# Kernel optimization log

Measured on AMD Instinct MI355X. Metric: run time of the kernel, lower is better.

## Reference

```python
import jax, jax.numpy as jnp
import numpy as np

N, E, IN_DIM, H, D = 40000, 640000, 128, 8, 16


def setup_inputs() -> dict:
    key = jax.random.key(0)
    k_h, k_s, k_d, k_q, k_k, k_v = jax.random.split(key, 6)
    scale = float(np.sqrt(2.0 / (IN_DIM + H * D)))  # xavier-ish
    return {
        "h": jax.random.normal(k_h, (N, IN_DIM), dtype=jnp.float32),
        "src": jax.random.randint(k_s, (E,), 0, N, dtype=jnp.int32),
        "dst": jax.random.randint(k_d, (E,), 0, N, dtype=jnp.int32),
        "WQ": jax.random.normal(k_q, (IN_DIM, H * D), dtype=jnp.float32) * scale,
        "WK": jax.random.normal(k_k, (IN_DIM, H * D), dtype=jnp.float32) * scale,
        "WV": jax.random.normal(k_v, (IN_DIM, H * D), dtype=jnp.float32) * scale,
    }


def reference(h, src, dst, WQ, WK, WV):
    n = h.shape[0]
    Q = (h @ WQ).reshape(n, H, D)  # [N,H,D]
    K = (h @ WK).reshape(n, H, D)
    V = (h @ WV).reshape(n, H, D)
    inv_sqrt_d = 1.0 / jnp.sqrt(jnp.asarray(D, dtype=h.dtype))
    # per-edge elementwise score (DGL u_mul_v keeps the H x D vector)
    score = K[src] * Q[dst] * inv_sqrt_d  # [E,H,D]
    wV = jax.ops.segment_sum(V[src] * score, dst, num_segments=n)  # [N,H,D]
    z = jax.ops.segment_sum(score, dst, num_segments=n)            # [N,H,D]
    return wV / (z + 1e-6)
```

## Files before the change

### kernel.cpp

```cpp
#include <hip/hip_runtime.h>


#define FMA4(acc, s, b) do { \
    (acc).x = fmaf((s), (b).x, (acc).x); \
    (acc).y = fmaf((s), (b).y, (acc).y); \
    (acc).z = fmaf((s), (b).z, (acc).z); \
    (acc).w = fmaf((s), (b).w, (acc).w); } while (0)

__global__ __launch_bounds__(256) void gemm_qkv(
    const float* __restrict__ h,
    const float* __restrict__ WQ,
    const float* __restrict__ WK,
    const float* __restrict__ WV,
    float* __restrict__ Qf,
    float* __restrict__ KV,
    int N)
{
    __shared__ float4 Wl[128 * 32];
    __shared__ float4 Hl[32 * 32];
    const int t = threadIdx.x;
    const int which = blockIdx.y;
    const float* Wsel = (which == 0) ? WQ : ((which == 1) ? WK : WV);
    const float4* W4 = (const float4*)Wsel;
#pragma unroll
    for (int i = 0; i < 16; ++i) Wl[t + i * 256] = W4[t + i * 256];

    const int c4 = t & 31;
    const int r4 = t >> 5;
    float4* Obase = (which == 0) ? (float4*)Qf : (float4*)KV;
    const int ostride = (which == 0) ? 32 : 64;
    const int ooff = (which == 2) ? 32 : 0;

    for (int sub = 0; sub < 4; ++sub) {
        const int r0 = (blockIdx.x * 4 + sub) * 32;
        if (r0 >= N) break;
        __syncthreads();
        const float4* H4 = (const float4*)(h + (size_t)r0 * 128);
#pragma unroll
        for (int i = 0; i < 4; ++i) Hl[t + i * 256] = H4[t + i * 256];
        __syncthreads();

        float4 acc0 = make_float4(0.f, 0.f, 0.f, 0.f);
        float4 acc1 = acc0, acc2 = acc0, acc3 = acc0;
#pragma unroll 8
        for (int k4 = 0; k4 < 32; ++k4) {
            float4 b0 = Wl[(k4 * 4 + 0) * 32 + c4];
            float4 b1 = Wl[(k4 * 4 + 1) * 32 + c4];
            float4 b2 = Wl[(k4 * 4 + 2) * 32 + c4];
            float4 b3 = Wl[(k4 * 4 + 3) * 32 + c4];
            float4 a0 = Hl[(r4 * 4 + 0) * 32 + k4];
            float4 a1 = Hl[(r4 * 4 + 1) * 32 + k4];
            float4 a2 = Hl[(r4 * 4 + 2) * 32 + k4];
            float4 a3 = Hl[(r4 * 4 + 3) * 32 + k4];
            FMA4(acc0, a0.x, b0); FMA4(acc0, a0.y, b1); FMA4(acc0, a0.z, b2); FMA4(acc0, a0.w, b3);
            FMA4(acc1, a1.x, b0); FMA4(acc1, a1.y, b1); FMA4(acc1, a1.z, b2); FMA4(acc1, a1.w, b3);
            FMA4(acc2, a2.x, b0); FMA4(acc2, a2.y, b1); FMA4(acc2, a2.z, b2); FMA4(acc2, a2.w, b3);
            FMA4(acc3, a3.x, b0); FMA4(acc3, a3.y, b1); FMA4(acc3, a3.z, b2); FMA4(acc3, a3.w, b3);
        }
        const int row = r0 + r4 * 4;
        Obase[(size_t)(row + 0) * ostride + ooff + c4] = acc0;
        Obase[(size_t)(row + 1) * ostride + ooff + c4] = acc1;
        Obase[(size_t)(row + 2) * ostride + ooff + c4] = acc2;
        Obase[(size_t)(row + 3) * ostride + ooff + c4] = acc3;
    }
}

__global__ __launch_bounds__(256) void count_deg(
    const int* __restrict__ dst, int* __restrict__ deg, int E)
{
    const int e = blockIdx.x * 256 + threadIdx.x;
    if (e < E) atomicAdd(&deg[dst[e]], 1);
}

__global__ __launch_bounds__(256) void chunk_reduce(
    const int* __restrict__ deg, int* __restrict__ csum, int N)
{
    const int t = threadIdx.x;
    const int i = blockIdx.x * 256 + t;
    int x = (i < N) ? deg[i] : 0;
#pragma unroll
    for (int off = 32; off; off >>= 1) x += __shfl_down(x, off, 64);
    __shared__ int ws[4];
    if ((t & 63) == 0) ws[t >> 6] = x;
    __syncthreads();
    if (t == 0) csum[blockIdx.x] = ws[0] + ws[1] + ws[2] + ws[3];
}

__global__ __launch_bounds__(256) void scan_chunks(
    const int* __restrict__ csum, int* __restrict__ coff, int nChunks)
{
    __shared__ int s[256];
    __shared__ int carry;
    const int t = threadIdx.x;
    if (t == 0) carry = 0;
    __syncthreads();
    for (int base = 0; base < nChunks; base += 256) {
        const int i = base + t;
        int x = (i < nChunks) ? csum[i] : 0;
        s[t] = x;
        __syncthreads();
        for (int off = 1; off < 256; off <<= 1) {
            int v = (t >= off) ? s[t - off] : 0;
            __syncthreads();
            s[t] += v;
            __syncthreads();
        }
        if (i < nChunks) coff[i] = carry + s[t] - x;
        __syncthreads();
        if (t == 0) carry += s[255];
        __syncthreads();
    }
}

__global__ __launch_bounds__(256) void chunk_scan(
    const int* __restrict__ deg, const int* __restrict__ coff,
    int* __restrict__ rowptr, int N)
{
    __shared__ int s[256];
    const int t = threadIdx.x;
    const int i = blockIdx.x * 256 + t;
    int x = (i < N) ? deg[i] : 0;
    s[t] = x;
    __syncthreads();
    for (int off = 1; off < 256; off <<= 1) {
        int v = (t >= off) ? s[t - off] : 0;
        __syncthreads();
        s[t] += v;
        __syncthreads();
    }
    if (i < N) rowptr[i + 1] = coff[blockIdx.x] + s[t];
    if (i == 0) rowptr[0] = 0;
}

__global__ __launch_bounds__(256) void scatter_pairs(
    const int* __restrict__ dst, const int* __restrict__ src,
    const int* __restrict__ rowptr, int* __restrict__ cur,
    int2* __restrict__ pairs, int E)
{
    const int e = blockIdx.x * 256 + threadIdx.x;
    if (e >= E) return;
    const int d = dst[e];
    const int pos = rowptr[d] + atomicAdd(&cur[d], 1);
    pairs[pos] = make_int2(e, src[e]);
}

__global__ __launch_bounds__(256) void sort_emit_srcs(
    const int* __restrict__ rowptr, int2* __restrict__ pairs,
    int* __restrict__ srcs, int N)
{
    const int n = blockIdx.x * 256 + threadIdx.x;
    if (n >= N) return;
    const int lo = rowptr[n], hi = rowptr[n + 1];
    for (int i = lo + 1; i < hi; ++i) {
        const int2 key = pairs[i];
        int j = i - 1;
        while (j >= lo && pairs[j].x > key.x) { pairs[j + 1] = pairs[j]; --j; }
        pairs[j + 1] = key;
    }
    for (int i = lo; i < hi; ++i) srcs[i] = pairs[i].y;
}

__global__ __launch_bounds__(64) void attn_out(
    const int* __restrict__ srcs, const int* __restrict__ rowptr,
    const float* __restrict__ KV, const float* __restrict__ Qf,
    float* __restrict__ out, int N)
{
#pragma clang fp contract(off)
    const int d = blockIdx.x;
    const int c = threadIdx.x;
    const float2 q = ((const float2*)Qf)[(size_t)d * 64 + c];
    const int lo = rowptr[d], hi = rowptr[d + 1];
    const float2* KV2 = (const float2*)KV;
    float2 z = make_float2(0.f, 0.f), wv = z;

#define EDGE_UPD(k, v) do { \
        float sc0 = ((k).x * q.x) * 0.25f; z.x = z.x + sc0; wv.x = wv.x + (v).x * sc0; \
        float sc1 = ((k).y * q.y) * 0.25f; z.y = z.y + sc1; wv.y = wv.y + (v).y * sc1; \
    } while (0)

    int i = lo;
    for (; i + 4 <= hi; i += 4) {
        const int s0 = srcs[i + 0], s1 = srcs[i + 1];
        const int s2 = srcs[i + 2], s3 = srcs[i + 3];
        const float2 k0 = KV2[(size_t)s0 * 128 + c], v0 = KV2[(size_t)s0 * 128 + 64 + c];
        const float2 k1 = KV2[(size_t)s1 * 128 + c], v1 = KV2[(size_t)s1 * 128 + 64 + c];
        const float2 k2 = KV2[(size_t)s2 * 128 + c], v2 = KV2[(size_t)s2 * 128 + 64 + c];
        const float2 k3 = KV2[(size_t)s3 * 128 + c], v3 = KV2[(size_t)s3 * 128 + 64 + c];
        EDGE_UPD(k0, v0); EDGE_UPD(k1, v1); EDGE_UPD(k2, v2); EDGE_UPD(k3, v3);
    }
    for (; i < hi; ++i) {
        const int s = srcs[i];
        const float2 k = KV2[(size_t)s * 128 + c], v = KV2[(size_t)s * 128 + 64 + c];
        EDGE_UPD(k, v);
    }
#undef EDGE_UPD

    float2 o;
    o.x = wv.x / (z.x + 1e-6f);
    o.y = wv.y / (z.y + 1e-6f);
    ((float2*)out)[(size_t)d * 64 + c] = o;
}

extern "C" void kernel_launch(void* const* d_in, const int* in_sizes, int n_in,
                              void* d_out, int out_size, void* d_ws, size_t ws_size,
                              hipStream_t stream)
{
    const float* h  = (const float*)d_in[0];
    const int* src  = (const int*)d_in[1];
    const int* dst  = (const int*)d_in[2];
    const float* WQ = (const float*)d_in[3];
    const float* WK = (const float*)d_in[4];
    const float* WV = (const float*)d_in[5];
    const int N = in_sizes[0] / 128;
    const int E = in_sizes[1];
    const size_t NC = (size_t)N * 128;
    const int nChunks = (N + 255) / 256;

    float* KV = (float*)d_ws;
    float* Qf = KV + (size_t)N * 256;
    int* deg    = (int*)(Qf + NC);
    int* cur    = deg + N;
    int* rowptr = cur + N;
    int* csum   = rowptr + (N + 1);
    int* coff   = csum + nChunks;
    int* srcs   = coff + nChunks;
    int2* pairs = (int2*)(srcs + E);
    float* outp = (float*)d_out;

    hipMemsetAsync(deg, 0, (size_t)2 * N * sizeof(int), stream);

    dim3 ggrid((N + 127) / 128, 3);
    gemm_qkv<<<ggrid, 256, 0, stream>>>(h, WQ, WK, WV, Qf, KV, N);

    const int eb = (E + 255) / 256;
    count_deg<<<eb, 256, 0, stream>>>(dst, deg, E);
    chunk_reduce<<<nChunks, 256, 0, stream>>>(deg, csum, N);
    scan_chunks<<<1, 256, 0, stream>>>(csum, coff, nChunks);
    chunk_scan<<<nChunks, 256, 0, stream>>>(deg, coff, rowptr, N);
    scatter_pairs<<<eb, 256, 0, stream>>>(dst, src, rowptr, cur, pairs, E);
    sort_emit_srcs<<<(N + 255) / 256, 256, 0, stream>>>(rowptr, pairs, srcs, N);

    attn_out<<<N, 64, 0, stream>>>(srcs, rowptr, KV, Qf, outp, N);
}
```

Baseline: 336.2 us.

## Retile QKV GEMM, rank-sort edges per wave, and batch gather loads

The QKV GEMM moves from a block that holds all of W in LDS and walks 4 row subtiles to a K-chunked 128-row tile with an 8x8 register block per thread, which cuts LDS footprint and raises arithmetic reuse per load. The per-node serial insertion sort becomes a wave-parallel rank sort using shuffles, with a single-lane fallback for degrees above 64. attn_out packs two nodes per 128-thread block and adds an 8-edge unrolled gather so more loads are in flight. Risks are higher register pressure in the GEMM and the slow serial fallback for high-degree nodes.

```diff
diff --git a/kernel.cpp b/kernel.cpp
--- a/kernel.cpp
+++ b/kernel.cpp
@@ -16,52 +16,73 @@
     float* __restrict__ KV,
     int N)
 {
-    __shared__ float4 Wl[128 * 32];
-    __shared__ float4 Hl[32 * 32];
+    __shared__ float4 Wl[32 * 32];
+    __shared__ float4 Hl[128 * 8];
     const int t = threadIdx.x;
     const int which = blockIdx.y;
     const float* Wsel = (which == 0) ? WQ : ((which == 1) ? WK : WV);
     const float4* W4 = (const float4*)Wsel;
-#pragma unroll
-    for (int i = 0; i < 16; ++i) Wl[t + i * 256] = W4[t + i * 256];
-
-    const int c4 = t & 31;
-    const int r4 = t >> 5;
+    const int r0 = blockIdx.x * 128;
+
+    const int tc = t & 15;
+    const int tr = t >> 4;
+
+    float4 acc[8][2];
+#pragma unroll
+    for (int i = 0; i < 8; ++i) {
+        acc[i][0] = make_float4(0.f, 0.f, 0.f, 0.f);
+        acc[i][1] = make_float4(0.f, 0.f, 0.f, 0.f);
+    }
+
+    for (int kc = 0; kc < 4; ++kc) {
+        __syncthreads();
+#pragma unroll
+        for (int i = 0; i < 4; ++i) {
+            const int idx = t + i * 256;
+            const int k = idx >> 5, c = idx & 31;
+            Wl[idx] = W4[(size_t)(kc * 32 + k) * 32 + c];
+        }
+#pragma unroll
+        for (int i = 0; i < 4; ++i) {
+            const int idx = t + i * 256;
+            const int row = idx >> 3, kk = idx & 7;
+            float4 v = make_float4(0.f, 0.f, 0.f, 0.f);
+            if (r0 + row < N)
+                v = ((const float4*)h)[(size_t)(r0 + row) * 32 + kc * 8 + kk];
+            Hl[row * 8 + kk] = v;
+        }
+        __syncthreads();
+
+        for (int k4 = 0; k4 < 8; ++k4) {
+            const float4 b0a = Wl[(k4 * 4 + 0) * 32 + tc * 2];
+            const float4 b0b = Wl[(k4 * 4 + 0) * 32 + tc * 2 + 1];
+            const float4 b1a = Wl[(k4 * 4 + 1) * 32 + tc * 2];
+            const float4 b1b = Wl[(k4 * 4 + 1) * 32 + tc * 2 + 1];
+            const float4 b2a = Wl[(k4 * 4 + 2) * 32 + tc * 2];
+            const float4 b2b = Wl[(k4 * 4 + 2) * 32 + tc * 2 + 1];
+            const float4 b3a = Wl[(k4 * 4 + 3) * 32 + tc * 2];
+            const float4 b3b = Wl[(k4 * 4 + 3) * 32 + tc * 2 + 1];
+#pragma unroll
+            for (int r = 0; r < 8; ++r) {
+                const float4 a = Hl[(tr * 8 + r) * 8 + k4];
+                FMA4(acc[r][0], a.x, b0a); FMA4(acc[r][1], a.x, b0b);
+                FMA4(acc[r][0], a.y, b1a); FMA4(acc[r][1], a.y, b1b);
+                FMA4(acc[r][0], a.z, b2a); FMA4(acc[r][1], a.z, b2b);
+                FMA4(acc[r][0], a.w, b3a); FMA4(acc[r][1], a.w, b3b);
+            }
+        }
+    }
+
     float4* Obase = (which == 0) ? (float4*)Qf : (float4*)KV;
     const int ostride = (which == 0) ? 32 : 64;
     const int ooff = (which == 2) ? 32 : 0;
-
-    for (int sub = 0; sub < 4; ++sub) {
-        const int r0 = (blockIdx.x * 4 + sub) * 32;
-        if (r0 >= N) break;
-        __syncthreads();
-        const float4* H4 = (const float4*)(h + (size_t)r0 * 128);
-#pragma unroll
-        for (int i = 0; i < 4; ++i) Hl[t + i * 256] = H4[t + i * 256];
-        __syncthreads();
-
-        float4 acc0 = make_float4(0.f, 0.f, 0.f, 0.f);
-        float4 acc1 = acc0, acc2 = acc0, acc3 = acc0;
-#pragma unroll 8
-        for (int k4 = 0; k4 < 32; ++k4) {
-            float4 b0 = Wl[(k4 * 4 + 0) * 32 + c4];
-            float4 b1 = Wl[(k4 * 4 + 1) * 32 + c4];
-            float4 b2 = Wl[(k4 * 4 + 2) * 32 + c4];
-            float4 b3 = Wl[(k4 * 4 + 3) * 32 + c4];
-            float4 a0 = Hl[(r4 * 4 + 0) * 32 + k4];
-            float4 a1 = Hl[(r4 * 4 + 1) * 32 + k4];
-            float4 a2 = Hl[(r4 * 4 + 2) * 32 + k4];
-            float4 a3 = Hl[(r4 * 4 + 3) * 32 + k4];
-            FMA4(acc0, a0.x, b0); FMA4(acc0, a0.y, b1); FMA4(acc0, a0.z, b2); FMA4(acc0, a0.w, b3);
-            FMA4(acc1, a1.x, b0); FMA4(acc1, a1.y, b1); FMA4(acc1, a1.z, b2); FMA4(acc1, a1.w, b3);
-            FMA4(acc2, a2.x, b0); FMA4(acc2, a2.y, b1); FMA4(acc2, a2.z, b2); FMA4(acc2, a2.w, b3);
-            FMA4(acc3, a3.x, b0); FMA4(acc3, a3.y, b1); FMA4(acc3, a3.z, b2); FMA4(acc3, a3.w, b3);
-        }
-        const int row = r0 + r4 * 4;
-        Obase[(size_t)(row + 0) * ostride + ooff + c4] = acc0;
-        Obase[(size_t)(row + 1) * ostride + ooff + c4] = acc1;
-        Obase[(size_t)(row + 2) * ostride + ooff + c4] = acc2;
-        Obase[(size_t)(row + 3) * ostride + ooff + c4] = acc3;
+#pragma unroll
+    for (int r = 0; r < 8; ++r) {
+        const int row = r0 + tr * 8 + r;
+        if (row < N) {
+            Obase[(size_t)row * ostride + ooff + tc * 2]     = acc[r][0];
+            Obase[(size_t)row * ostride + ooff + tc * 2 + 1] = acc[r][1];
+        }
     }
 }
 
@@ -144,31 +165,46 @@
     pairs[pos] = make_int2(e, src[e]);
 }
 
-__global__ __launch_bounds__(256) void sort_emit_srcs(
-    const int* __restrict__ rowptr, int2* __restrict__ pairs,
+__global__ __launch_bounds__(256) void rank_emit(
+    const int* __restrict__ rowptr, const int2* __restrict__ pairs,
     int* __restrict__ srcs, int N)
 {
-    const int n = blockIdx.x * 256 + threadIdx.x;
-    if (n >= N) return;
-    const int lo = rowptr[n], hi = rowptr[n + 1];
-    for (int i = lo + 1; i < hi; ++i) {
-        const int2 key = pairs[i];
-        int j = i - 1;
-        while (j >= lo && pairs[j].x > key.x) { pairs[j + 1] = pairs[j]; --j; }
-        pairs[j + 1] = key;
-    }
-    for (int i = lo; i < hi; ++i) srcs[i] = pairs[i].y;
-}
-
-__global__ __launch_bounds__(64) void attn_out(
+    const int wave = threadIdx.x >> 6;
+    const int lane = threadIdx.x & 63;
+    const int d = blockIdx.x * 4 + wave;
+    if (d >= N) return;
+    const int lo = rowptr[d];
+    const int deg = rowptr[d + 1] - lo;
+    if (deg <= 64) {
+        int2 p = make_int2(0x7fffffff, 0);
+        if (lane < deg) p = pairs[lo + lane];
+        int rank = 0;
+        for (int j = 0; j < deg; ++j) {
+            const int kj = __shfl(p.x, j, 64);
+            rank += (kj < p.x) ? 1 : 0;
+        }
+        if (lane < deg) srcs[lo + rank] = p.y;
+    } else if (lane == 0) {
+        for (int i = 0; i < deg; ++i) {
+            const int2 pi = pairs[lo + i];
+            int rank = 0;
+            for (int j = 0; j < deg; ++j) rank += (pairs[lo + j].x < pi.x) ? 1 : 0;
+            srcs[lo + rank] = pi.y;
+        }
+    }
+}
+
+__global__ __launch_bounds__(128) void attn_out(
     const int* __restrict__ srcs, const int* __restrict__ rowptr,
     const float* __restrict__ KV, const float* __restrict__ Qf,
     float* __restrict__ out, int N)
 {
 #pragma clang fp contract(off)
-    const int d = blockIdx.x;
-    const int c = threadIdx.x;
-    const float2 q = ((const float2*)Qf)[(size_t)d * 64 + c];
+    const int wave = threadIdx.x >> 6;
+    const int lane = threadIdx.x & 63;
+    const int d = blockIdx.x * 2 + wave;
+    if (d >= N) return;
+    const float2 q = ((const float2*)Qf)[(size_t)d * 64 + lane];
     const int lo = rowptr[d], hi = rowptr[d + 1];
     const float2* KV2 = (const float2*)KV;
     float2 z = make_float2(0.f, 0.f), wv = z;
@@ -179,18 +215,31 @@
     } while (0)
 
     int i = lo;
+    for (; i + 8 <= hi; i += 8) {
+        int s[8];
+#pragma unroll
+        for (int u = 0; u < 8; ++u) s[u] = srcs[i + u];
+        float2 kk[8], vv[8];
+#pragma unroll
+        for (int u = 0; u < 8; ++u) {
+            kk[u] = KV2[(size_t)s[u] * 128 + lane];
+            vv[u] = KV2[(size_t)s[u] * 128 + 64 + lane];
+        }
+#pragma unroll
+        for (int u = 0; u < 8; ++u) EDGE_UPD(kk[u], vv[u]);
+    }
     for (; i + 4 <= hi; i += 4) {
         const int s0 = srcs[i + 0], s1 = srcs[i + 1];
         const int s2 = srcs[i + 2], s3 = srcs[i + 3];
-        const float2 k0 = KV2[(size_t)s0 * 128 + c], v0 = KV2[(size_t)s0 * 128 + 64 + c];
-        const float2 k1 = KV2[(size_t)s1 * 128 + c], v1 = KV2[(size_t)s1 * 128 + 64 + c];
-        const float2 k2 = KV2[(size_t)s2 * 128 + c], v2 = KV2[(size_t)s2 * 128 + 64 + c];
-        const float2 k3 = KV2[(size_t)s3 * 128 + c], v3 = KV2[(size_t)s3 * 128 + 64 + c];
+        const float2 k0 = KV2[(size_t)s0 * 128 + lane], v0 = KV2[(size_t)s0 * 128 + 64 + lane];
+        const float2 k1 = KV2[(size_t)s1 * 128 + lane], v1 = KV2[(size_t)s1 * 128 + 64 + lane];
+        const float2 k2 = KV2[(size_t)s2 * 128 + lane], v2 = KV2[(size_t)s2 * 128 + 64 + lane];
+        const float2 k3 = KV2[(size_t)s3 * 128 + lane], v3 = KV2[(size_t)s3 * 128 + 64 + lane];
         EDGE_UPD(k0, v0); EDGE_UPD(k1, v1); EDGE_UPD(k2, v2); EDGE_UPD(k3, v3);
     }
     for (; i < hi; ++i) {
         const int s = srcs[i];
-        const float2 k = KV2[(size_t)s * 128 + c], v = KV2[(size_t)s * 128 + 64 + c];
+        const float2 k = KV2[(size_t)s * 128 + lane], v = KV2[(size_t)s * 128 + 64 + lane];
         EDGE_UPD(k, v);
     }
 #undef EDGE_UPD
@@ -198,7 +247,7 @@
     float2 o;
     o.x = wv.x / (z.x + 1e-6f);
     o.y = wv.y / (z.y + 1e-6f);
-    ((float2*)out)[(size_t)d * 64 + c] = o;
+    ((float2*)out)[(size_t)d * 64 + lane] = o;
 }
 
 extern "C" void kernel_launch(void* const* d_in, const int* in_sizes, int n_in,
@@ -221,7 +270,7 @@
     int* deg    = (int*)(Qf + NC);
     int* cur    = deg + N;
     int* rowptr = cur + N;
-    int* csum   = rowptr + (N + 1);
+    int* csum   = rowptr + (N + 2);
     int* coff   = csum + nChunks;
     int* srcs   = coff + nChunks;
     int2* pairs = (int2*)(srcs + E);
@@ -238,7 +287,7 @@
     scan_chunks<<<1, 256, 0, stream>>>(csum, coff, nChunks);
     chunk_scan<<<nChunks, 256, 0, stream>>>(deg, coff, rowptr, N);
     scatter_pairs<<<eb, 256, 0, stream>>>(dst, src, rowptr, cur, pairs, E);
-    sort_emit_srcs<<<(N + 255) / 256, 256, 0, stream>>>(rowptr, pairs, srcs, N);
-
-    attn_out<<<N, 64, 0, stream>>>(srcs, rowptr, KV, Qf, outp, N);
-}
+    rank_emit<<<(N + 3) / 4, 256, 0, stream>>>(rowptr, pairs, srcs, N);
+
+    attn_out<<<(N + 1) / 2, 128, 0, stream>>>(srcs, rowptr, KV, Qf, outp, N);
+}
```

Result: faster. 302.1 us (-10.2%).
